# Optimization experiments

Hardware: AMD Instinct MI355X
Metric: run time of the kernel (lower is better)

## Reference

```python
import jax, jax.numpy as jnp
import numpy as np

B, T, D_IN, H, G = 64, 512, 862, 1024, 4096  # G = 4*H, PyTorch gate order i,f,g,o


def setup_inputs() -> dict:
    key = jax.random.key(0)
    ks = jax.random.split(key, 9)
    s0 = 1.0 / np.sqrt(H)  # PyTorch LSTM init scale
    return {
        "x": jax.random.normal(ks[0], (B, T, D_IN), dtype=jnp.float32),
        "W_ih0": jax.random.normal(ks[1], (G, D_IN), dtype=jnp.float32) * s0,
        "W_hh0": jax.random.normal(ks[2], (G, H), dtype=jnp.float32) * s0,
        "b_ih0": jax.random.normal(ks[3], (G,), dtype=jnp.float32) * s0,
        "b_hh0": jax.random.normal(ks[4], (G,), dtype=jnp.float32) * s0,
        "W_ih1": jax.random.normal(ks[5], (G, H), dtype=jnp.float32) * s0,
        "W_hh1": jax.random.normal(ks[6], (G, H), dtype=jnp.float32) * s0,
        "b_ih1": jax.random.normal(ks[7], (G,), dtype=jnp.float32) * s0,
        "b_hh1": jax.random.normal(ks[8], (G,), dtype=jnp.float32) * s0,
    }


def _lstm_layer(x, W_ih, W_hh, b_ih, b_hh):
    # x: [B, T, D]; gates precomputed for the input projection (one big GEMM)
    b, t, _ = x.shape
    h_dim = W_hh.shape[1]
    xg = jnp.einsum("btd,gd->btg", x, W_ih) + (b_ih + b_hh)  # [B, T, 4H]

    def step(carry, xt):
        h, c = carry
        g = xt + h @ W_hh.T  # [B, 4H]
        i, f, gc, o = jnp.split(g, 4, axis=-1)  # PyTorch order i,f,g,o
        i = jax.nn.sigmoid(i)
        f = jax.nn.sigmoid(f)
        gc = jnp.tanh(gc)
        o = jax.nn.sigmoid(o)
        c = f * c + i * gc
        h = o * jnp.tanh(c)
        return (h, c), h

    h0 = jnp.zeros((b, h_dim), x.dtype)
    c0 = jnp.zeros((b, h_dim), x.dtype)
    _, hs = jax.lax.scan(step, (h0, c0), jnp.swapaxes(xg, 0, 1))  # [T, B, H]
    return jnp.swapaxes(hs, 0, 1)  # [B, T, H]


def reference(x, W_ih0, W_hh0, b_ih0, b_hh0, W_ih1, W_hh1, b_ih1, b_hh1):
    h1 = _lstm_layer(x, W_ih0, W_hh0, b_ih0, b_hh0)
    out = _lstm_layer(h1, W_ih1, W_hh1, b_ih1, b_hh1)
    return out
```

## Files before the change

kernel.cpp:

```cpp
#include <hip/hip_runtime.h>
#include <cstdint>

#define BATCH 64
#define SEQ   512
#define DIN   862
#define DPAD  896
#define HID   1024
#define NG    4096

typedef _Float16 f16;
typedef __attribute__((ext_vector_type(8))) _Float16 f16x8;
typedef __attribute__((ext_vector_type(4))) float    f32x4;

__device__ __forceinline__ void glds16(const f16* g, f16* l) {
    auto gp = (const __attribute__((address_space(1))) void*)(uintptr_t)g;
    auto lp = (__attribute__((address_space(3))) void*)(uint32_t)(uintptr_t)l;
    __builtin_amdgcn_global_load_lds(gp, lp, 16, 0, 0);
}

__device__ __forceinline__ float sigf(float x) {
    return __builtin_amdgcn_rcpf(1.f + __expf(-x));
}
__device__ __forceinline__ float tanh_fast(float x) {
    float xx = fminf(15.f, fmaxf(-15.f, x));
    float e = __expf(2.f * xx);
    return (e - 1.f) * __builtin_amdgcn_rcpf(e + 1.f);
}

__device__ __forceinline__ long xg_index(int t, int b, int n) {
    int bs = b >> 4, bl = b & 15;
    int g = n >> 10, jh = n & 1023;
    int jg = jh >> 4, jl = jh & 15;
    return (((((long)t * 4 + bs) * 64 + jg) * 4 + g) * 16 + bl) * 16 + jl;
}

__global__ __launch_bounds__(256) void prep_kernel(
    const float* __restrict__ x,
    const float* __restrict__ Wih0, const float* __restrict__ Whh0,
    const float* __restrict__ bih0, const float* __restrict__ bhh0,
    const float* __restrict__ Wih1, const float* __restrict__ Whh1,
    const float* __restrict__ bih1, const float* __restrict__ bhh1,
    f16* __restrict__ xh, f16* __restrict__ W0h, f16* __restrict__ Wh0h,
    f16* __restrict__ W1h, f16* __restrict__ Wh1h,
    float* __restrict__ b0, float* __restrict__ b1, unsigned* __restrict__ bar)
{
    long tid = (long)blockIdx.x * blockDim.x + threadIdx.x;
    long np  = (long)gridDim.x * blockDim.x;
    for (long i = tid; i < (long)BATCH * SEQ * DPAD; i += np) {
        long m = i / DPAD, k = i % DPAD;
        xh[i] = (k < DIN) ? (f16)x[m * DIN + k] : (f16)0.f;
    }
    for (long i = tid; i < (long)NG * DPAD; i += np) {
        long n = i / DPAD, k = i % DPAD;
        W0h[i] = (k < DIN) ? (f16)Wih0[n * DIN + k] : (f16)0.f;
    }
    for (long i = tid; i < (long)NG * HID; i += np) {
        Wh0h[i] = (f16)Whh0[i];
        W1h[i]  = (f16)Wih1[i];
        Wh1h[i] = (f16)Whh1[i];
    }
    for (long i = tid; i < NG; i += np) { b0[i] = bih0[i] + bhh0[i]; b1[i] = bih1[i] + bhh1[i]; }
    for (long i = tid; i < 2048; i += np) bar[i] = 0u;
}

__global__ __launch_bounds__(256) void gemm_f16(
    const f16* __restrict__ A, const f16* __restrict__ Bw,
    const float* __restrict__ bias, f16* __restrict__ out, int K, int mode)
{
    __shared__ f16 smem[2 * 128 * 32];
    const int tid  = threadIdx.x;
    const int lane = tid & 63, wave = tid >> 6;
    const int wm = wave >> 1, wn = wave & 1;
    const int quad = lane >> 4, l15 = lane & 15;
    const int bm = blockIdx.x >> 5, bn = blockIdx.x & 31;
    const long m0 = (long)bm * 128, n0 = (long)bn * 128;
    const int r4 = lane >> 2, g4 = lane & 3;

    f32x4 acc[4][4];
#pragma unroll
    for (int i = 0; i < 4; ++i)
#pragma unroll
        for (int j = 0; j < 4; ++j)
#pragma unroll
            for (int r = 0; r < 4; ++r) acc[i][j][r] = 0.f;

#pragma unroll 1
    for (int kk = 0; kk < K; kk += 32) {
#pragma unroll
        for (int c = 0; c < 2; ++c) {
            int idx = wave * 2 + c;
            int lr  = idx * 16 + r4;
            int gs  = g4 ^ ((lr >> 1) & 3);
            glds16(A  + (m0 + lr) * (long)K + kk + gs * 8, smem + idx * 512);
            glds16(Bw + (n0 + lr) * (long)K + kk + gs * 8, smem + 4096 + idx * 512);
        }
        __syncthreads();
        f16x8 af[4], bf[4];
#pragma unroll
        for (int i = 0; i < 4; ++i) {
            int lr = 64 * wm + 16 * i + l15;
            int sl = quad ^ ((lr >> 1) & 3);
            af[i] = *(const f16x8*)(smem + lr * 32 + sl * 8);
        }
#pragma unroll
        for (int j = 0; j < 4; ++j) {
            int lr = 64 * wn + 16 * j + l15;
            int sl = quad ^ ((lr >> 1) & 3);
            bf[j] = *(const f16x8*)(smem + 4096 + lr * 32 + sl * 8);
        }
#pragma unroll
        for (int i = 0; i < 4; ++i)
#pragma unroll
            for (int j = 0; j < 4; ++j)
                acc[i][j] = __builtin_amdgcn_mfma_f32_16x16x32_f16(af[i], bf[j], acc[i][j], 0, 0, 0);
        __syncthreads();
    }

#pragma unroll
    for (int j = 0; j < 4; ++j) {
        int n = (int)n0 + 64 * wn + 16 * j + l15;
        float bv = bias[n];
#pragma unroll
        for (int i = 0; i < 4; ++i) {
#pragma unroll
            for (int r = 0; r < 4; ++r) {
                int m = (int)m0 + 64 * wm + 16 * i + quad * 4 + r;
                int t, b;
                if (mode == 1) { b = m >> 9; t = m & 511; }
                else           { t = m >> 6; b = m & 63; }
                out[xg_index(t, b, n)] = (f16)(acc[i][j][r] + bv);
            }
        }
    }
}

__device__ __forceinline__ void grid_barrier_nf(unsigned* bar, unsigned target) {
    asm volatile("s_waitcnt vmcnt(0)" ::: "memory");
    __syncthreads();
    if (threadIdx.x == 0) {
        unsigned grp = blockIdx.x >> 4;
        unsigned prev = __hip_atomic_fetch_add(&bar[grp * 32], 1u, __ATOMIC_RELAXED, __HIP_MEMORY_SCOPE_AGENT);
        if ((prev & 15u) == 15u) {
            unsigned pr = __hip_atomic_fetch_add(&bar[512], 1u, __ATOMIC_RELAXED, __HIP_MEMORY_SCOPE_AGENT);
            if ((pr & 15u) == 15u)
                __hip_atomic_store(&bar[544], target, __ATOMIC_RELAXED, __HIP_MEMORY_SCOPE_AGENT);
        }
        while (__hip_atomic_load(&bar[544], __ATOMIC_RELAXED, __HIP_MEMORY_SCOPE_AGENT) < target)
            __builtin_amdgcn_s_sleep(1);
    }
    __syncthreads();
}

__global__ __launch_bounds__(256, 1) void lstm_layer(
    const f16* __restrict__ xg, const f16* __restrict__ Whh,
    f16* __restrict__ hseq, float* __restrict__ out32, unsigned* __restrict__ bar)
{
    __shared__ float P[4 * 4 * 16 * 17];
    const int tid = threadIdx.x;
    const int lane = tid & 63, w = tid >> 6;
    const int quad = lane >> 4, l15 = lane & 15;
    const int bs = blockIdx.x & 3;
    const int jg = blockIdx.x >> 2;
    const int ks0 = 256 * w;

    f16x8 wf[4][8];
#pragma unroll
    for (int g = 0; g < 4; ++g) {
        const f16* Wp = Whh + ((long)g * HID + jg * 16 + l15) * HID + ks0 + quad * 8;
#pragma unroll
        for (int s = 0; s < 8; ++s)
            wf[g][s] = *(const f16x8*)(Wp + s * 32);
    }
#pragma unroll
    for (int g = 0; g < 4; ++g)
#pragma unroll
        for (int s = 0; s < 8; ++s)
            asm volatile("" : "+v"(wf[g][s]));

    const int gb = tid >> 4, gj = tid & 15;
    const int bG = bs * 16 + gb, jG = jg * 16 + gj;
    unsigned* hw = (unsigned*)hseq;
    float cst = 0.f;

#pragma unroll 1
    for (int t = 0; t < SEQ; ++t) {
        const f16* xp = xg + (((long)t * 4 + bs) * 64 + jg) * 1024 + gb * 16 + gj;
        float xgi = (float)xp[0];
        float xgf = (float)xp[256];
        float xgg = (float)xp[512];
        float xgo = (float)xp[768];

        f32x4 acc[4];
#pragma unroll
        for (int g = 0; g < 4; ++g)
#pragma unroll
            for (int r = 0; r < 4; ++r) acc[g][r] = 0.f;

        if (t > 0) {
            const unsigned long long* hp = (const unsigned long long*)
                (hseq + ((long)(t - 1) * BATCH + bs * 16 + l15) * HID + ks0 + quad * 8);
#pragma unroll
            for (int s = 0; s < 8; ++s) {
                union { unsigned long long u[2]; f16x8 v; } af;
                af.u[0] = __hip_atomic_load((unsigned long long*)(hp + s * 8),
                                            __ATOMIC_RELAXED, __HIP_MEMORY_SCOPE_AGENT);
                af.u[1] = __hip_atomic_load((unsigned long long*)(hp + s * 8 + 1),
                                            __ATOMIC_RELAXED, __HIP_MEMORY_SCOPE_AGENT);
#pragma unroll
                for (int g = 0; g < 4; ++g)
                    acc[g] = __builtin_amdgcn_mfma_f32_16x16x32_f16(af.v, wf[g][s], acc[g], 0, 0, 0);
            }
        }

#pragma unroll
        for (int g = 0; g < 4; ++g)
#pragma unroll
            for (int r = 0; r < 4; ++r)
                P[((w * 4 + g) * 16 + quad * 4 + r) * 17 + l15] = acc[g][r];
        __syncthreads();

        float gate[4];
#pragma unroll
        for (int g = 0; g < 4; ++g) {
            float s0 = P[((0 * 4 + g) * 16 + gb) * 17 + gj];
            float s1 = P[((1 * 4 + g) * 16 + gb) * 17 + gj];
            float s2 = P[((2 * 4 + g) * 16 + gb) * 17 + gj];
            float s3 = P[((3 * 4 + g) * 16 + gb) * 17 + gj];
            gate[g] = (s0 + s1) + (s2 + s3);
        }

        float gi = gate[0] + xgi;
        float gf = gate[1] + xgf;
        float gg = gate[2] + xgg;
        float go = gate[3] + xgo;
        float si = sigf(gi), sf = sigf(gf), so = sigf(go);
        float tg = tanh_fast(gg);
        cst = sf * cst + si * tg;
        float h = so * tanh_fast(cst);

        union { f16 f; unsigned short u; } cv; cv.f = (f16)h;
        unsigned hv = cv.u;
        unsigned ov = __shfl_xor(hv, 1);
        if (!(tid & 1))
            __hip_atomic_store(&hw[(((long)t * BATCH + bG) * HID + jG) >> 1],
                               hv | (ov << 16), __ATOMIC_RELAXED, __HIP_MEMORY_SCOPE_AGENT);
        if (out32) out32[((long)bG * SEQ + t) * HID + jG] = h;

        if (t + 1 < SEQ) grid_barrier_nf(bar, (unsigned)(t + 1));
    }
}

extern "C" void kernel_launch(void* const* d_in, const int* in_sizes, int n_in,
                              void* d_out, int out_size, void* d_ws, size_t ws_size,
                              hipStream_t stream) {
    (void)in_sizes; (void)n_in; (void)out_size; (void)ws_size;
    const float* x    = (const float*)d_in[0];
    const float* Wih0 = (const float*)d_in[1];
    const float* Whh0 = (const float*)d_in[2];
    const float* bih0 = (const float*)d_in[3];
    const float* bhh0 = (const float*)d_in[4];
    const float* Wih1 = (const float*)d_in[5];
    const float* Whh1 = (const float*)d_in[6];
    const float* bih1 = (const float*)d_in[7];
    const float* bhh1 = (const float*)d_in[8];

    char* ws = (char*)d_ws;
    size_t off = 0;
    auto alloc = [&](size_t bytes) { char* p = ws + off; off += (bytes + 255) & ~(size_t)255; return p; };
    f16*   XG   = (f16*)alloc((size_t)SEQ * BATCH * NG * 2);
    f16*   xh   = (f16*)alloc((size_t)BATCH * SEQ * DPAD * 2);
    f16*   h1   = (f16*)alloc((size_t)SEQ * BATCH * HID * 2);
    f16*   W0h  = (f16*)alloc((size_t)NG * DPAD * 2);
    f16*   Wh0h = (f16*)alloc((size_t)NG * HID * 2);
    f16*   W1h  = (f16*)alloc((size_t)NG * HID * 2);
    f16*   Wh1h = (f16*)alloc((size_t)NG * HID * 2);
    float* b0   = (float*)alloc((size_t)NG * 4);
    float* b1   = (float*)alloc((size_t)NG * 4);
    unsigned* bar = (unsigned*)alloc(2048 * 4);

    prep_kernel<<<dim3(2048), dim3(256), 0, stream>>>(x, Wih0, Whh0, bih0, bhh0,
                                                      Wih1, Whh1, bih1, bhh1,
                                                      xh, W0h, Wh0h, W1h, Wh1h, b0, b1, bar);

    gemm_f16<<<dim3(8192), dim3(256), 0, stream>>>(xh, W0h, b0, XG, DPAD, 1);

    {
        const f16* xgp = XG; const f16* whp = Wh0h; f16* hp = h1;
        float* op = nullptr; unsigned* bp = bar;
        void* args[] = { (void*)&xgp, (void*)&whp, (void*)&hp, (void*)&op, (void*)&bp };
        (void)hipLaunchCooperativeKernel((const void*)lstm_layer, dim3(256), dim3(256), args, 0, stream);
    }

    gemm_f16<<<dim3(8192), dim3(256), 0, stream>>>(h1, W1h, b1, XG, HID, 2);

    {
        const f16* xgp = XG; const f16* whp = Wh1h; f16* hp = h1;
        float* op = (float*)d_out; unsigned* bp = bar + 1024;
        void* args[] = { (void*)&xgp, (void*)&whp, (void*)&hp, (void*)&op, (void*)&bp };
        (void)hipLaunchCooperativeKernel((const void*)lstm_layer, dim3(256), dim3(256), args, 0, stream);
    }
}
```

Measured before the change: 6.046 ms.

## Fuse both LSTM layers into one wavefront-pipelined cooperative kernel

Replaces the two sequential per-layer recurrent kernels and the layer-1 input GEMM with a single cooperative kernel of 512 blocks. Half the blocks run layer 0 and half run layer 1, which consumes h1[t] as soon as it is ready, so the two recurrences overlap in a wavefront. Layer-1 blocks compute the input projection inline, streaming W_ih1 fragments from memory every step. The global grid barrier is replaced by per-batch-slice leaf counters that each wave increments and consumers poll, so dependencies are tracked per batch group. This needs two blocks resident per CU and adds per-step W_ih1 reloads, with a fallback to the old path if occupancy is insufficient.

```diff
diff --git a/kernel.cpp b/kernel.cpp
--- a/kernel.cpp
+++ b/kernel.cpp
@@ -11,6 +11,7 @@
 typedef _Float16 f16;
 typedef __attribute__((ext_vector_type(8))) _Float16 f16x8;
 typedef __attribute__((ext_vector_type(4))) float    f32x4;
+typedef unsigned long long u64;
 
 __device__ __forceinline__ void glds16(const f16* g, f16* l) {
     auto gp = (const __attribute__((address_space(1))) void*)(uintptr_t)g;
@@ -32,6 +33,19 @@
     int g = n >> 10, jh = n & 1023;
     int jg = jh >> 4, jl = jh & 15;
     return (((((long)t * 4 + bs) * 64 + jg) * 4 + g) * 16 + bl) * 16 + jl;
+}
+
+__device__ __forceinline__ unsigned leaf_load(const unsigned* p) {
+    return __hip_atomic_load((unsigned*)p, __ATOMIC_RELAXED, __HIP_MEMORY_SCOPE_AGENT);
+}
+__device__ __forceinline__ void leaf_add(unsigned* p) {
+    __hip_atomic_fetch_add(p, 1u, __ATOMIC_RELAXED, __HIP_MEMORY_SCOPE_AGENT);
+}
+__device__ __forceinline__ f16x8 h_frag_load(const f16* p) {
+    union { u64 u[2]; f16x8 v; } r;
+    r.u[0] = __hip_atomic_load((u64*)p,     __ATOMIC_RELAXED, __HIP_MEMORY_SCOPE_AGENT);
+    r.u[1] = __hip_atomic_load((u64*)p + 1, __ATOMIC_RELAXED, __HIP_MEMORY_SCOPE_AGENT);
+    return r.v;
 }
 
 __global__ __launch_bounds__(256) void prep_kernel(
@@ -60,7 +74,7 @@
         Wh1h[i] = (f16)Whh1[i];
     }
     for (long i = tid; i < NG; i += np) { b0[i] = bih0[i] + bhh0[i]; b1[i] = bih1[i] + bhh1[i]; }
-    for (long i = tid; i < 2048; i += np) bar[i] = 0u;
+    for (long i = tid; i < 8192; i += np) bar[i] = 0u;
 }
 
 __global__ __launch_bounds__(256) void gemm_f16(
@@ -134,6 +148,228 @@
     }
 }
 
+#define IH_STEP(SS, CURB)                                                                   \
+    {                                                                                       \
+        _Pragma("unroll") for (int g = 0; g < 4; ++g)                                       \
+            acc[g] = __builtin_amdgcn_mfma_f32_16x16x32_f16(af1[SS], CURB[g], acc[g], 0, 0, 0); \
+        if (t > 0) {                                                                        \
+            _Pragma("unroll") for (int g = 0; g < 4; ++g)                                   \
+                acc[g] = __builtin_amdgcn_mfma_f32_16x16x32_f16(af2[SS], wf[g][SS], acc[g], 0, 0, 0); \
+        }                                                                                   \
+        if (SS < 6) {                                                                       \
+            _Pragma("unroll") for (int g = 0; g < 4; ++g)                                   \
+                CURB[g] = *(const f16x8*)(wbase[g] + (SS + 2) * 32);                        \
+        }                                                                                   \
+    }
+
+__global__ __launch_bounds__(256, 2) void lstm_fused(
+    const f16* __restrict__ xg1, const f16* __restrict__ Whh0,
+    const f16* __restrict__ W1,  const f16* __restrict__ Whh1,
+    const float* __restrict__ b1,
+    f16* __restrict__ bufA, f16* __restrict__ bufB,
+    float* __restrict__ out32, unsigned* __restrict__ bar)
+{
+    __shared__ float P[4 * 4 * 16 * 17];
+    const int tid = threadIdx.x;
+    const int lane = tid & 63, w = tid >> 6;
+    const int quad = lane >> 4, l15 = lane & 15;
+    const bool roleB = (blockIdx.x >= 256);
+    const int idx = roleB ? (int)blockIdx.x - 256 : (int)blockIdx.x;
+    const int bs = idx & 3, jg = idx >> 2;
+    const int ks0 = 256 * w;
+    unsigned* leavesA = bar + bs * 512;
+    unsigned* leavesB = bar + 2048 + bs * 512;
+    unsigned* myLeaf = (roleB ? leavesB : leavesA) + (((jg << 2) | w) & 15) * 32;
+    const int gb = tid >> 4, gj = tid & 15;
+    const int bG = bs * 16 + gb, jG = jg * 16 + gj;
+
+    if (!roleB) {
+        f16x8 wf[4][8];
+#pragma unroll
+        for (int g = 0; g < 4; ++g) {
+            const f16* Wp = Whh0 + ((long)g * HID + jg * 16 + l15) * HID + ks0 + quad * 8;
+#pragma unroll
+            for (int s = 0; s < 8; ++s) wf[g][s] = *(const f16x8*)(Wp + s * 32);
+        }
+#pragma unroll
+        for (int g = 0; g < 4; ++g)
+#pragma unroll
+            for (int s = 0; s < 8; ++s) asm volatile("" : "+v"(wf[g][s]));
+
+        unsigned* hwA = (unsigned*)bufA;
+        float cst = 0.f;
+        const f16* xq = xg1 + (((long)0 * 4 + bs) * 64 + jg) * 1024 + gb * 16 + gj;
+        f16 xr0 = xq[0], xr1 = xq[256], xr2 = xq[512], xr3 = xq[768];
+
+#pragma unroll 1
+        for (int t = 0; t < SEQ; ++t) {
+            if (t > 0) {
+                unsigned tgt = 16u * (unsigned)t;
+                const unsigned* pp = leavesA + (lane & 15) * 32;
+                for (;;) {
+                    unsigned v = (lane < 16) ? leaf_load(pp) : tgt;
+                    if (__all((int)(v >= tgt))) break;
+                    __builtin_amdgcn_s_sleep(1);
+                }
+            }
+            f32x4 acc[4];
+#pragma unroll
+            for (int g = 0; g < 4; ++g)
+#pragma unroll
+                for (int r = 0; r < 4; ++r) acc[g][r] = 0.f;
+
+            if (t > 0) {
+                const f16* hp = bufA + ((long)(t - 1) * BATCH + bs * 16 + l15) * HID + ks0 + quad * 8;
+                f16x8 af[8];
+#pragma unroll
+                for (int s = 0; s < 8; ++s) af[s] = h_frag_load(hp + s * 32);
+#pragma unroll
+                for (int s = 0; s < 8; ++s)
+#pragma unroll
+                    for (int g = 0; g < 4; ++g)
+                        acc[g] = __builtin_amdgcn_mfma_f32_16x16x32_f16(af[s], wf[g][s], acc[g], 0, 0, 0);
+            }
+
+#pragma unroll
+            for (int g = 0; g < 4; ++g)
+#pragma unroll
+                for (int r = 0; r < 4; ++r)
+                    P[((w * 4 + g) * 16 + quad * 4 + r) * 17 + l15] = acc[g][r];
+            __syncthreads();
+
+            float gate[4];
+#pragma unroll
+            for (int g = 0; g < 4; ++g) {
+                float s0 = P[((0 * 4 + g) * 16 + gb) * 17 + gj];
+                float s1 = P[((1 * 4 + g) * 16 + gb) * 17 + gj];
+                float s2 = P[((2 * 4 + g) * 16 + gb) * 17 + gj];
+                float s3 = P[((3 * 4 + g) * 16 + gb) * 17 + gj];
+                gate[g] = (s0 + s1) + (s2 + s3);
+            }
+            float gi = gate[0] + (float)xr0;
+            float gf = gate[1] + (float)xr1;
+            float gg = gate[2] + (float)xr2;
+            float go = gate[3] + (float)xr3;
+            float si = sigf(gi), sf = sigf(gf), so = sigf(go);
+            float tg = tanh_fast(gg);
+            cst = sf * cst + si * tg;
+            float h = so * tanh_fast(cst);
+
+            union { f16 f; unsigned short u; } cv; cv.f = (f16)h;
+            unsigned hv = cv.u;
+            unsigned ov = __shfl_xor(hv, 1);
+            if (!(tid & 1))
+                __hip_atomic_store(&hwA[(((long)t * BATCH + bG) * HID + jG) >> 1],
+                                   hv | (ov << 16), __ATOMIC_RELAXED, __HIP_MEMORY_SCOPE_AGENT);
+            asm volatile("s_waitcnt vmcnt(0)" ::: "memory");
+            if (lane == 0) leaf_add(myLeaf);
+            if (t + 1 < SEQ) {
+                const f16* xn = xg1 + (((long)(t + 1) * 4 + bs) * 64 + jg) * 1024 + gb * 16 + gj;
+                xr0 = xn[0]; xr1 = xn[256]; xr2 = xn[512]; xr3 = xn[768];
+            }
+        }
+    } else {
+        f16x8 wf[4][8];
+#pragma unroll
+        for (int g = 0; g < 4; ++g) {
+            const f16* Wp = Whh1 + ((long)g * HID + jg * 16 + l15) * HID + ks0 + quad * 8;
+#pragma unroll
+            for (int s = 0; s < 8; ++s) wf[g][s] = *(const f16x8*)(Wp + s * 32);
+        }
+#pragma unroll
+        for (int g = 0; g < 4; ++g)
+#pragma unroll
+            for (int s = 0; s < 8; ++s) asm volatile("" : "+v"(wf[g][s]));
+
+        float b1v[4];
+#pragma unroll
+        for (int g = 0; g < 4; ++g) b1v[g] = b1[g * HID + jG];
+        const f16* wbase[4];
+#pragma unroll
+        for (int g = 0; g < 4; ++g)
+            wbase[g] = W1 + ((long)g * HID + jg * 16 + l15) * HID + ks0 + quad * 8;
+        f16x8 ihA[4], ihB[4];
+#pragma unroll
+        for (int g = 0; g < 4; ++g) ihA[g] = *(const f16x8*)(wbase[g]);
+#pragma unroll
+        for (int g = 0; g < 4; ++g) ihB[g] = *(const f16x8*)(wbase[g] + 32);
+
+        unsigned* hwB = (unsigned*)bufB;
+        float cst = 0.f;
+
+#pragma unroll 1
+        for (int t = 0; t < SEQ; ++t) {
+            {
+                unsigned tgtA = 16u * (unsigned)(t + 1), tgtB = 16u * (unsigned)t;
+                int nact = (t > 0) ? 32 : 16;
+                const unsigned* pp = (lane < 16) ? (leavesA + lane * 32)
+                                                 : (leavesB + (lane & 15) * 32);
+                unsigned tgt = (lane < 16) ? tgtA : tgtB;
+                for (;;) {
+                    unsigned v = (lane < nact) ? leaf_load(pp) : tgt;
+                    if (__all((int)(v >= tgt))) break;
+                    __builtin_amdgcn_s_sleep(1);
+                }
+            }
+            f32x4 acc[4];
+#pragma unroll
+            for (int g = 0; g < 4; ++g)
+#pragma unroll
+                for (int r = 0; r < 4; ++r) acc[g][r] = 0.f;
+
+            const f16* hp1 = bufA + ((long)t * BATCH + bs * 16 + l15) * HID + ks0 + quad * 8;
+            f16x8 af1[8];
+#pragma unroll
+            for (int s = 0; s < 8; ++s) af1[s] = h_frag_load(hp1 + s * 32);
+            f16x8 af2[8];
+            if (t > 0) {
+                const f16* hp2 = bufB + ((long)(t - 1) * BATCH + bs * 16 + l15) * HID + ks0 + quad * 8;
+#pragma unroll
+                for (int s = 0; s < 8; ++s) af2[s] = h_frag_load(hp2 + s * 32);
+            }
+            IH_STEP(0, ihA) IH_STEP(1, ihB) IH_STEP(2, ihA) IH_STEP(3, ihB)
+            IH_STEP(4, ihA) IH_STEP(5, ihB) IH_STEP(6, ihA) IH_STEP(7, ihB)
+
+#pragma unroll
+            for (int g = 0; g < 4; ++g)
+#pragma unroll
+                for (int r = 0; r < 4; ++r)
+                    P[((w * 4 + g) * 16 + quad * 4 + r) * 17 + l15] = acc[g][r];
+            __syncthreads();
+
+            float gate[4];
+#pragma unroll
+            for (int g = 0; g < 4; ++g) {
+                float s0 = P[((0 * 4 + g) * 16 + gb) * 17 + gj];
+                float s1 = P[((1 * 4 + g) * 16 + gb) * 17 + gj];
+                float s2 = P[((2 * 4 + g) * 16 + gb) * 17 + gj];
+                float s3 = P[((3 * 4 + g) * 16 + gb) * 17 + gj];
+                gate[g] = ((s0 + s1) + (s2 + s3)) + b1v[g];
+            }
+            float si = sigf(gate[0]), sf = sigf(gate[1]), so = sigf(gate[3]);
+            float tg = tanh_fast(gate[2]);
+            cst = sf * cst + si * tg;
+            float h = so * tanh_fast(cst);
+
+            union { f16 f; unsigned short u; } cv; cv.f = (f16)h;
+            unsigned hv = cv.u;
+            unsigned ov = __shfl_xor(hv, 1);
+            if (!(tid & 1))
+                __hip_atomic_store(&hwB[(((long)t * BATCH + bG) * HID + jG) >> 1],
+                                   hv | (ov << 16), __ATOMIC_RELAXED, __HIP_MEMORY_SCOPE_AGENT);
+            out32[((long)bG * SEQ + t) * HID + jG] = h;
+            asm volatile("s_waitcnt vmcnt(0)" ::: "memory");
+            if (lane == 0) leaf_add(myLeaf);
+            if (t + 1 < SEQ) {
+#pragma unroll
+                for (int g = 0; g < 4; ++g) ihA[g] = *(const f16x8*)(wbase[g]);
+#pragma unroll
+                for (int g = 0; g < 4; ++g) ihB[g] = *(const f16x8*)(wbase[g] + 32);
+            }
+        }
+    }
+}
+
 __device__ __forceinline__ void grid_barrier_nf(unsigned* bar, unsigned target) {
     asm volatile("s_waitcnt vmcnt(0)" ::: "memory");
     __syncthreads();
@@ -168,14 +404,12 @@
     for (int g = 0; g < 4; ++g) {
         const f16* Wp = Whh + ((long)g * HID + jg * 16 + l15) * HID + ks0 + quad * 8;
 #pragma unroll
-        for (int s = 0; s < 8; ++s)
-            wf[g][s] = *(const f16x8*)(Wp + s * 32);
+        for (int s = 0; s < 8; ++s) wf[g][s] = *(const f16x8*)(Wp + s * 32);
     }
 #pragma unroll
     for (int g = 0; g < 4; ++g)
 #pragma unroll
-        for (int s = 0; s < 8; ++s)
-            asm volatile("" : "+v"(wf[g][s]));
+        for (int s = 0; s < 8; ++s) asm volatile("" : "+v"(wf[g][s]));
 
     const int gb = tid >> 4, gj = tid & 15;
     const int bG = bs * 16 + gb, jG = jg * 16 + gj;
@@ -197,18 +431,13 @@
             for (int r = 0; r < 4; ++r) acc[g][r] = 0.f;
 
         if (t > 0) {
-            const unsigned long long* hp = (const unsigned long long*)
-                (hseq + ((long)(t - 1) * BATCH + bs * 16 + l15) * HID + ks0 + quad * 8);
+            const f16* hp = hseq + ((long)(t - 1) * BATCH + bs * 16 + l15) * HID + ks0 + quad * 8;
 #pragma unroll
             for (int s = 0; s < 8; ++s) {
-                union { unsigned long long u[2]; f16x8 v; } af;
-                af.u[0] = __hip_atomic_load((unsigned long long*)(hp + s * 8),
-                                            __ATOMIC_RELAXED, __HIP_MEMORY_SCOPE_AGENT);
-                af.u[1] = __hip_atomic_load((unsigned long long*)(hp + s * 8 + 1),
-                                            __ATOMIC_RELAXED, __HIP_MEMORY_SCOPE_AGENT);
+                f16x8 af = h_frag_load(hp + s * 32);
 #pragma unroll
                 for (int g = 0; g < 4; ++g)
-                    acc[g] = __builtin_amdgcn_mfma_f32_16x16x32_f16(af.v, wf[g][s], acc[g], 0, 0, 0);
+                    acc[g] = __builtin_amdgcn_mfma_f32_16x16x32_f16(af, wf[g][s], acc[g], 0, 0, 0);
             }
         }
 
@@ -253,7 +482,7 @@
 extern "C" void kernel_launch(void* const* d_in, const int* in_sizes, int n_in,
                               void* d_out, int out_size, void* d_ws, size_t ws_size,
                               hipStream_t stream) {
-    (void)in_sizes; (void)n_in; (void)out_size; (void)ws_size;
+    (void)in_sizes; (void)n_in; (void)out_size;
     const float* x    = (const float*)d_in[0];
     const float* Wih0 = (const float*)d_in[1];
     const float* Whh0 = (const float*)d_in[2];
@@ -276,7 +505,9 @@
     f16*   Wh1h = (f16*)alloc((size_t)NG * HID * 2);
     float* b0   = (float*)alloc((size_t)NG * 4);
     float* b1   = (float*)alloc((size_t)NG * 4);
-    unsigned* bar = (unsigned*)alloc(2048 * 4);
+    unsigned* bar = (unsigned*)alloc(8192 * 4);
+    f16*   h2   = (f16*)alloc((size_t)SEQ * BATCH * HID * 2);
+    size_t need = off;
 
     prep_kernel<<<dim3(2048), dim3(256), 0, stream>>>(x, Wih0, Whh0, bih0, bhh0,
                                                       Wih1, Whh1, bih1, bhh1,
@@ -284,19 +515,31 @@
 
     gemm_f16<<<dim3(8192), dim3(256), 0, stream>>>(xh, W0h, b0, XG, DPAD, 1);
 
-    {
-        const f16* xgp = XG; const f16* whp = Wh0h; f16* hp = h1;
-        float* op = nullptr; unsigned* bp = bar;
-        void* args[] = { (void*)&xgp, (void*)&whp, (void*)&hp, (void*)&op, (void*)&bp };
-        (void)hipLaunchCooperativeKernel((const void*)lstm_layer, dim3(256), dim3(256), args, 0, stream);
-    }
-
-    gemm_f16<<<dim3(8192), dim3(256), 0, stream>>>(h1, W1h, b1, XG, HID, 2);
-
-    {
-        const f16* xgp = XG; const f16* whp = Wh1h; f16* hp = h1;
-        float* op = (float*)d_out; unsigned* bp = bar + 1024;
-        void* args[] = { (void*)&xgp, (void*)&whp, (void*)&hp, (void*)&op, (void*)&bp };
-        (void)hipLaunchCooperativeKernel((const void*)lstm_layer, dim3(256), dim3(256), args, 0, stream);
-    }
-}
+    int occ = 0;
+    (void)hipOccupancyMaxActiveBlocksPerMultiprocessor(&occ, (const void*)lstm_fused, 256, 0);
+    bool fused_ok = (occ >= 2) && (ws_size == 0 || ws_size >= need);
+    if (fused_ok) {
+        const f16* xgp = XG; const f16* w0p = Wh0h; const f16* w1p = W1h; const f16* wh1p = Wh1h;
+        const float* b1p = b1; f16* bA = h1; f16* bB = h2;
+        float* op = (float*)d_out; unsigned* bp = bar;
+        void* args[] = { (void*)&xgp, (void*)&w0p, (void*)&w1p, (void*)&wh1p,
+                         (void*)&b1p, (void*)&bA, (void*)&bB, (void*)&op, (void*)&bp };
+        hipError_t e = hipLaunchCooperativeKernel((const void*)lstm_fused, dim3(512), dim3(256), args, 0, stream);
+        fused_ok = (e == hipSuccess);
+    }
+    if (!fused_ok) {
+        {
+            const f16* xgp = XG; const f16* whp = Wh0h; f16* hp = h1;
+            float* op = nullptr; unsigned* bp = bar;
+            void* args[] = { (void*)&xgp, (void*)&whp, (void*)&hp, (void*)&op, (void*)&bp };
+            (void)hipLaunchCooperativeKernel((const void*)lstm_layer, dim3(256), dim3(256), args, 0, stream);
+        }
+        gemm_f16<<<dim3(8192), dim3(256), 0, stream>>>(h1, W1h, b1, XG, HID, 2);
+        {
+            const f16* xgp = XG; const f16* whp = Wh1h; f16* hp = h1;
+            float* op = (float*)d_out; unsigned* bp = bar + 1024;
+            void* args[] = { (void*)&xgp, (void*)&whp, (void*)&hp, (void*)&op, (void*)&bp };
+            (void)hipLaunchCooperativeKernel((const void*)lstm_layer, dim3(256), dim3(256), args, 0, stream);
+        }
+    }
+}
```

Result: no change. 6.054 ms (+0.1%).

## Replace grid barrier with poisoned hidden-state dataflow polling in LSTM recurrence

Applied to the files above, without the earlier changes.

Removes the per-timestep grid-wide barrier and instead pre-fills hidden-state buffers with a poison pattern. Each block spins on its own h(t-1) slice until no word holds the poison value. Each block then waits only for the data it needs rather than for all blocks, which removes the two-level atomic barrier latency from every step. Layer 2 gets its own h buffer so layer 1 outputs are not overwritten. In exchange, prep must now write two full poison buffers, every step polls with atomics, and the correctness argument relies on a valid packed fp16 pair never equaling 0xFFFFFFFF (a NaN pattern).

```diff
diff --git a/kernel.cpp b/kernel.cpp
--- a/kernel.cpp
+++ b/kernel.cpp
@@ -7,10 +7,12 @@
 #define DPAD  896
 #define HID   1024
 #define NG    4096
+#define POIS  0xFFFFFFFFu
 
 typedef _Float16 f16;
 typedef __attribute__((ext_vector_type(8))) _Float16 f16x8;
 typedef __attribute__((ext_vector_type(4))) float    f32x4;
+typedef unsigned long long u64;
 
 __device__ __forceinline__ void glds16(const f16* g, f16* l) {
     auto gp = (const __attribute__((address_space(1))) void*)(uintptr_t)g;
@@ -42,7 +44,8 @@
     const float* __restrict__ bih1, const float* __restrict__ bhh1,
     f16* __restrict__ xh, f16* __restrict__ W0h, f16* __restrict__ Wh0h,
     f16* __restrict__ W1h, f16* __restrict__ Wh1h,
-    float* __restrict__ b0, float* __restrict__ b1, unsigned* __restrict__ bar)
+    float* __restrict__ b0, float* __restrict__ b1,
+    unsigned* __restrict__ h1p, unsigned* __restrict__ h2p)
 {
     long tid = (long)blockIdx.x * blockDim.x + threadIdx.x;
     long np  = (long)gridDim.x * blockDim.x;
@@ -60,7 +63,11 @@
         Wh1h[i] = (f16)Whh1[i];
     }
     for (long i = tid; i < NG; i += np) { b0[i] = bih0[i] + bhh0[i]; b1[i] = bih1[i] + bhh1[i]; }
-    for (long i = tid; i < 2048; i += np) bar[i] = 0u;
+    const long HW = (long)SEQ * BATCH * HID / 2;
+    for (long i = tid; i < HW; i += np) {
+        __hip_atomic_store(&h1p[i], POIS, __ATOMIC_RELAXED, __HIP_MEMORY_SCOPE_AGENT);
+        __hip_atomic_store(&h2p[i], POIS, __ATOMIC_RELAXED, __HIP_MEMORY_SCOPE_AGENT);
+    }
 }
 
 __global__ __launch_bounds__(256) void gemm_f16(
@@ -134,26 +141,9 @@
     }
 }
 
-__device__ __forceinline__ void grid_barrier_nf(unsigned* bar, unsigned target) {
-    asm volatile("s_waitcnt vmcnt(0)" ::: "memory");
-    __syncthreads();
-    if (threadIdx.x == 0) {
-        unsigned grp = blockIdx.x >> 4;
-        unsigned prev = __hip_atomic_fetch_add(&bar[grp * 32], 1u, __ATOMIC_RELAXED, __HIP_MEMORY_SCOPE_AGENT);
-        if ((prev & 15u) == 15u) {
-            unsigned pr = __hip_atomic_fetch_add(&bar[512], 1u, __ATOMIC_RELAXED, __HIP_MEMORY_SCOPE_AGENT);
-            if ((pr & 15u) == 15u)
-                __hip_atomic_store(&bar[544], target, __ATOMIC_RELAXED, __HIP_MEMORY_SCOPE_AGENT);
-        }
-        while (__hip_atomic_load(&bar[544], __ATOMIC_RELAXED, __HIP_MEMORY_SCOPE_AGENT) < target)
-            __builtin_amdgcn_s_sleep(1);
-    }
-    __syncthreads();
-}
-
 __global__ __launch_bounds__(256, 1) void lstm_layer(
     const f16* __restrict__ xg, const f16* __restrict__ Whh,
-    f16* __restrict__ hseq, float* __restrict__ out32, unsigned* __restrict__ bar)
+    f16* __restrict__ hseq, float* __restrict__ out32)
 {
     __shared__ float P[4 * 4 * 16 * 17];
     const int tid = threadIdx.x;
@@ -197,19 +187,31 @@
             for (int r = 0; r < 4; ++r) acc[g][r] = 0.f;
 
         if (t > 0) {
-            const unsigned long long* hp = (const unsigned long long*)
-                (hseq + ((long)(t - 1) * BATCH + bs * 16 + l15) * HID + ks0 + quad * 8);
-#pragma unroll
-            for (int s = 0; s < 8; ++s) {
-                union { unsigned long long u[2]; f16x8 v; } af;
-                af.u[0] = __hip_atomic_load((unsigned long long*)(hp + s * 8),
-                                            __ATOMIC_RELAXED, __HIP_MEMORY_SCOPE_AGENT);
-                af.u[1] = __hip_atomic_load((unsigned long long*)(hp + s * 8 + 1),
-                                            __ATOMIC_RELAXED, __HIP_MEMORY_SCOPE_AGENT);
+            const f16* hpf = hseq + ((long)(t - 1) * BATCH + bs * 16 + l15) * HID + ks0 + quad * 8;
+            f16x8 af[8];
+            for (;;) {
+                bool ok = true;
+#pragma unroll
+                for (int s = 0; s < 8; ++s) {
+                    const u64* p = (const u64*)(hpf + s * 32);
+                    u64 a = __hip_atomic_load((u64*)p,
+                                              __ATOMIC_RELAXED, __HIP_MEMORY_SCOPE_AGENT);
+                    u64 b = __hip_atomic_load((u64*)p + 1,
+                                              __ATOMIC_RELAXED, __HIP_MEMORY_SCOPE_AGENT);
+                    ok = ok && ((unsigned)a != POIS) && ((unsigned)(a >> 32) != POIS)
+                            && ((unsigned)b != POIS) && ((unsigned)(b >> 32) != POIS);
+                    union { u64 u[2]; f16x8 v; } cv2;
+                    cv2.u[0] = a; cv2.u[1] = b;
+                    af[s] = cv2.v;
+                }
+                if (__all((int)ok)) break;
+                __builtin_amdgcn_s_sleep(1);
+            }
+#pragma unroll
+            for (int s = 0; s < 8; ++s)
 #pragma unroll
                 for (int g = 0; g < 4; ++g)
-                    acc[g] = __builtin_amdgcn_mfma_f32_16x16x32_f16(af.v, wf[g][s], acc[g], 0, 0, 0);
-            }
+                    acc[g] = __builtin_amdgcn_mfma_f32_16x16x32_f16(af[s], wf[g][s], acc[g], 0, 0, 0);
         }
 
 #pragma unroll
@@ -228,6 +230,7 @@
             float s3 = P[((3 * 4 + g) * 16 + gb) * 17 + gj];
             gate[g] = (s0 + s1) + (s2 + s3);
         }
+        __syncthreads();
 
         float gi = gate[0] + xgi;
         float gf = gate[1] + xgf;
@@ -245,8 +248,6 @@
             __hip_atomic_store(&hw[(((long)t * BATCH + bG) * HID + jG) >> 1],
                                hv | (ov << 16), __ATOMIC_RELAXED, __HIP_MEMORY_SCOPE_AGENT);
         if (out32) out32[((long)bG * SEQ + t) * HID + jG] = h;
-
-        if (t + 1 < SEQ) grid_barrier_nf(bar, (unsigned)(t + 1));
     }
 }
 
@@ -270,33 +271,32 @@
     f16*   XG   = (f16*)alloc((size_t)SEQ * BATCH * NG * 2);
     f16*   xh   = (f16*)alloc((size_t)BATCH * SEQ * DPAD * 2);
     f16*   h1   = (f16*)alloc((size_t)SEQ * BATCH * HID * 2);
+    f16*   h2   = (f16*)alloc((size_t)SEQ * BATCH * HID * 2);
     f16*   W0h  = (f16*)alloc((size_t)NG * DPAD * 2);
     f16*   Wh0h = (f16*)alloc((size_t)NG * HID * 2);
     f16*   W1h  = (f16*)alloc((size_t)NG * HID * 2);
     f16*   Wh1h = (f16*)alloc((size_t)NG * HID * 2);
     float* b0   = (float*)alloc((size_t)NG * 4);
     float* b1   = (float*)alloc((size_t)NG * 4);
-    unsigned* bar = (unsigned*)alloc(2048 * 4);
 
     prep_kernel<<<dim3(2048), dim3(256), 0, stream>>>(x, Wih0, Whh0, bih0, bhh0,
                                                       Wih1, Whh1, bih1, bhh1,
-                                                      xh, W0h, Wh0h, W1h, Wh1h, b0, b1, bar);
+                                                      xh, W0h, Wh0h, W1h, Wh1h, b0, b1,
+                                                      (unsigned*)h1, (unsigned*)h2);
 
     gemm_f16<<<dim3(8192), dim3(256), 0, stream>>>(xh, W0h, b0, XG, DPAD, 1);
 
     {
-        const f16* xgp = XG; const f16* whp = Wh0h; f16* hp = h1;
-        float* op = nullptr; unsigned* bp = bar;
-        void* args[] = { (void*)&xgp, (void*)&whp, (void*)&hp, (void*)&op, (void*)&bp };
+        const f16* xgp = XG; const f16* whp = Wh0h; f16* hp = h1; float* op = nullptr;
+        void* args[] = { (void*)&xgp, (void*)&whp, (void*)&hp, (void*)&op };
         (void)hipLaunchCooperativeKernel((const void*)lstm_layer, dim3(256), dim3(256), args, 0, stream);
     }
 
     gemm_f16<<<dim3(8192), dim3(256), 0, stream>>>(h1, W1h, b1, XG, HID, 2);
 
     {
-        const f16* xgp = XG; const f16* whp = Wh1h; f16* hp = h1;
-        float* op = (float*)d_out; unsigned* bp = bar + 1024;
-        void* args[] = { (void*)&xgp, (void*)&whp, (void*)&hp, (void*)&op, (void*)&bp };
+        const f16* xgp = XG; const f16* whp = Wh1h; f16* hp = h2; float* op = (float*)d_out;
+        void* args[] = { (void*)&xgp, (void*)&whp, (void*)&hp, (void*)&op };
         (void)hipLaunchCooperativeKernel((const void*)lstm_layer, dim3(256), dim3(256), args, 0, stream);
     }
 }
```

New measurement: 6.428 ms. 1.06x slower.
